# Optimization experiments

Measured on AMD Instinct MI355X. Metric: run time of the kernel, lower is better.

Reference implementation:

```python
import jax, jax.numpy as jnp
import numpy as np
from jax import lax

N, D, H = 4096, 256, 4


def setup_inputs() -> dict:
    key = jax.random.key(0)
    ks = jax.random.split(key, 6)
    x = jax.random.normal(ks[0], (1, 1, N, D), dtype=jnp.float32)
    adj = jax.random.randint(ks[1], (N, N), 0, 2, dtype=jnp.int32)
    conv_w = jax.random.normal(ks[2], (1, 1, 1, 1), dtype=jnp.float32)
    conv_b = jax.random.normal(ks[3], (1,), dtype=jnp.float32)
    # xavier_uniform on (H, 2D, 1) with gain 1.414
    limit = 1.414 * np.sqrt(6.0 / (2 * D + 1))
    a = jax.random.uniform(ks[4], (H, 2 * D, 1), minval=-limit, maxval=limit, dtype=jnp.float32)
    bias = jnp.zeros((D,), dtype=jnp.float32)
    return {"x": x, "adj": adj, "conv_w": conv_w, "conv_b": conv_b, "a": a, "bias": bias}


def reference(x, adj, conv_w, conv_b, a, bias):
    # 1x1 conv (NCHW / OIHW), preserves spatial dims
    h = lax.conv_general_dilated(x, conv_w, (1, 1), 'VALID',
                                 dimension_numbers=('NCHW', 'OIHW', 'NCHW'))
    h = h + conv_b[None, :, None, None]
    h = h[0, 0]                      # [N, D]
    d = h.shape[1]
    a1 = a[:, :d, 0]                 # [H, D]
    a2 = a[:, d:, 0]                 # [H, D]
    Wh1 = h @ a1.T                   # [N, H]
    Wh2 = h @ a2.T                   # [N, H]
    # e[k, i, j] = elu(Wh1[i, k] + Wh2[j, k])
    e = jax.nn.elu(Wh1.T[:, :, None] + Wh2.T[:, None, :])   # [H, N, N]
    att = jnp.where((adj > 0)[None, :, :], e, jnp.float32(-9e15))
    att = jax.nn.softmax(att, axis=-1)
    # dropout is inactive in eval mode (self.training=False)
    h_pass = jnp.einsum('hij,jd->hid', att, h).mean(axis=0)  # [N, D]
    out = jax.nn.elu(0.5 * h_pass + 0.5 * h)
    norm = jnp.maximum(jnp.linalg.norm(out, axis=1, keepdims=True), 1e-12)
    out = out / norm
    return out + bias
```

## Files before the change

kernel.cpp:

```cpp
#include <hip/hip_runtime.h>
#include <math.h>

#define NN 4096
#define DD 256
#define HH 4
#define SPLIT 8
#define BKG 64

typedef short short8 __attribute__((ext_vector_type(8)));
typedef float float4v __attribute__((ext_vector_type(4)));

__device__ __forceinline__ unsigned short f2bf(float f) {
  unsigned u = __float_as_uint(f);
  u += 0x7FFF + ((u >> 16) & 1);
  return (unsigned short)(u >> 16);
}
__device__ __forceinline__ unsigned f2bf_pk(float a, float b) {
  unsigned ua = __float_as_uint(a); ua += 0x7FFF + ((ua >> 16) & 1);
  unsigned ub = __float_as_uint(b); ub += 0x7FFF + ((ub >> 16) & 1);
  return __builtin_amdgcn_perm(ub, ua, 0x07060302);
}
__device__ __forceinline__ void gld16(void* lds, const void* gp) {
  __builtin_amdgcn_global_load_lds(
      (const __attribute__((address_space(1))) unsigned int*)gp,
      (__attribute__((address_space(3))) unsigned int*)lds, 16, 0, 0);
}

__global__ void k_zero(float* __restrict__ hp) {
  int idx = blockIdx.x * 256 + threadIdx.x;
  ((float4*)hp)[idx] = make_float4(0.f, 0.f, 0.f, 0.f);
}

__global__ __launch_bounds__(256) void k_pre(
    const float* __restrict__ x, const float* __restrict__ a,
    const float* __restrict__ cwp, const float* __restrict__ cbp,
    unsigned short* __restrict__ hbfT, float* __restrict__ Rpg,
    unsigned short* __restrict__ Ebf) {
  const int tid = threadIdx.x;
  const int bid = blockIdx.x;
  const float cw = cwp[0], cb = cbp[0];

  if (bid < 256) {
    __shared__ float t[64][65];
    const int j0 = (bid & 63) * 64, d0 = (bid >> 6) * 64;
    const int r = tid >> 4, c4 = tid & 15;
#pragma unroll
    for (int p = 0; p < 4; p++) {
      const int jj = p * 16 + r;
      const float4 v = *(const float4*)(x + (size_t)(j0 + jj) * DD + d0 + c4 * 4);
      t[jj][c4 * 4 + 0] = v.x * cw + cb;
      t[jj][c4 * 4 + 1] = v.y * cw + cb;
      t[jj][c4 * 4 + 2] = v.z * cw + cb;
      t[jj][c4 * 4 + 3] = v.w * cw + cb;
    }
    __syncthreads();
    const int jc = (tid & 15) * 4, db = tid >> 4;
#pragma unroll
    for (int p = 0; p < 4; p++) {
      const int dd = p * 16 + db;
      const unsigned l0 = f2bf(t[jc + 0][dd]);
      const unsigned l1 = f2bf(t[jc + 1][dd]);
      const unsigned l2 = f2bf(t[jc + 2][dd]);
      const unsigned l3 = f2bf(t[jc + 3][dd]);
      uint2 val;
      val.x = l0 | (l1 << 16);
      val.y = l2 | (l3 << 16);
      *(uint2*)(hbfT + (size_t)(d0 + dd) * NN + j0 + jc) = val;
    }
  } else {
    const int ln = tid >> 2, qd = (tid & 3) * 64;
    const int node = (bid - 256) * 64 + ln;
    float p1[HH] = {0.f, 0.f, 0.f, 0.f}, p2[HH] = {0.f, 0.f, 0.f, 0.f};
#pragma unroll
    for (int k = 0; k < 16; k++) {
      const int d = qd + k * 4;
      const float4 v = *(const float4*)(x + (size_t)node * DD + d);
      const float h0 = v.x * cw + cb, h1 = v.y * cw + cb;
      const float h2 = v.z * cw + cb, h3 = v.w * cw + cb;
#pragma unroll
      for (int h = 0; h < HH; h++) {
        const float4 a1 = *(const float4*)(a + h * 512 + d);
        const float4 a2 = *(const float4*)(a + h * 512 + 256 + d);
        p1[h] += h0 * a1.x + h1 * a1.y + h2 * a1.z + h3 * a1.w;
        p2[h] += h0 * a2.x + h1 * a2.y + h2 * a2.z + h3 * a2.w;
      }
    }
#pragma unroll
    for (int off = 1; off <= 2; off <<= 1) {
#pragma unroll
      for (int h = 0; h < HH; h++) {
        p1[h] += __shfl_xor(p1[h], off);
        p2[h] += __shfl_xor(p2[h], off);
      }
    }
    if ((tid & 3) == 0) {
#pragma unroll
      for (int h = 0; h < HH; h++) {
        Rpg[h * NN + node] = __expf(p1[h]);
        Ebf[h * NN + node] = f2bf(__expf(p2[h]));
      }
    }
  }
}

__global__ __launch_bounds__(256) void k_zw(
    const int* __restrict__ adj, const float* __restrict__ Rpg,
    const unsigned short* __restrict__ Ebf, unsigned short* __restrict__ Wm) {
  __shared__ float red[4][HH];
  __shared__ float sZi[HH];

  const int i = blockIdx.x;
  const int tid = threadIdx.x;
  const float C = 0.36787944117144233f;
  float Rp[HH], z[HH];
#pragma unroll
  for (int h = 0; h < HH; h++) {
    Rp[h] = Rpg[h * NN + i];
    z[h] = 0.f;
  }
  unsigned P[4][HH][2];
  const int4* arow = (const int4*)(adj + (size_t)i * NN);
#pragma unroll
  for (int k = 0; k < 4; k++) {
    const int j4 = tid + k * 256;
    const int4 av = arow[j4];
    const bool m0 = av.x > 0, m1 = av.y > 0, m2 = av.z > 0, m3 = av.w > 0;
#pragma unroll
    for (int h = 0; h < HH; h++) {
      const uint2 e2 = *(const uint2*)(Ebf + (size_t)h * NN + j4 * 4);
      const float E0 = __uint_as_float(e2.x << 16);
      const float E1 = __uint_as_float(e2.x & 0xffff0000u);
      const float E2 = __uint_as_float(e2.y << 16);
      const float E3 = __uint_as_float(e2.y & 0xffff0000u);
      float u, p0, p1, p2, p3;
      u = Rp[h] * E0; p0 = u > 1.f ? u : C * __expf(u);
      p0 = m0 ? p0 : 0.f;
      u = Rp[h] * E1; p1 = u > 1.f ? u : C * __expf(u);
      p1 = m1 ? p1 : 0.f;
      u = Rp[h] * E2; p2 = u > 1.f ? u : C * __expf(u);
      p2 = m2 ? p2 : 0.f;
      u = Rp[h] * E3; p3 = u > 1.f ? u : C * __expf(u);
      p3 = m3 ? p3 : 0.f;
      z[h] += (p0 + p1) + (p2 + p3);
      P[k][h][0] = f2bf_pk(p0, p1);
      P[k][h][1] = f2bf_pk(p2, p3);
    }
  }
#pragma unroll
  for (int h = 0; h < HH; h++) {
#pragma unroll
    for (int off = 32; off; off >>= 1) z[h] += __shfl_xor(z[h], off);
  }
  const int lane = tid & 63, wv = tid >> 6;
  if (lane == 0) {
#pragma unroll
    for (int h = 0; h < HH; h++) red[wv][h] = z[h];
  }
  __syncthreads();
  if (tid < HH) {
    const float zt = red[0][tid] + red[1][tid] + red[2][tid] + red[3][tid];
    sZi[tid] = zt > 0.f ? 0.25f / zt : 0.f;
  }
  __syncthreads();
  float Zi[HH];
#pragma unroll
  for (int h = 0; h < HH; h++) Zi[h] = sZi[h];

  unsigned* wrow = (unsigned*)(Wm + (size_t)i * NN);
#pragma unroll
  for (int k = 0; k < 4; k++) {
    const int j4 = tid + k * 256;
    float w0 = 0.f, w1 = 0.f, w2 = 0.f, w3 = 0.f;
#pragma unroll
    for (int h = 0; h < HH; h++) {
      const unsigned pa = P[k][h][0];
      const unsigned pb = P[k][h][1];
      w0 += __uint_as_float(pa << 16) * Zi[h];
      w1 += __uint_as_float(pa & 0xffff0000u) * Zi[h];
      w2 += __uint_as_float(pb << 16) * Zi[h];
      w3 += __uint_as_float(pb & 0xffff0000u) * Zi[h];
    }
    wrow[j4 * 2] = f2bf_pk(w0, w1);
    wrow[j4 * 2 + 1] = f2bf_pk(w2, w3);
  }
}

__global__ __launch_bounds__(256) void k_gemm(
    const unsigned short* __restrict__ Wm, const unsigned short* __restrict__ hbfT,
    float* __restrict__ hpOut, int useSplit) {
  __shared__ __align__(16) unsigned short sA[64 * 64];
  __shared__ __align__(16) unsigned short sB[256 * 64];
  const int tid = threadIdx.x;
  const int wv = tid >> 6, lane = tid & 63;
  const int m16 = lane & 15, q = lane >> 4, m7 = m16 & 7;
  const int rb = blockIdx.x >> 3, sp = blockIdx.x & 7;
  const int i0 = rb * 64;
  const int jlo = sp * (NN / SPLIT);
  const int lr = lane >> 3;
  const int lk8 = (lane & 7) ^ lr;

  float4v acc[4][4];
#pragma unroll
  for (int a = 0; a < 4; a++)
#pragma unroll
    for (int b = 0; b < 4; b++) acc[a][b] = (float4v)0.f;

  for (int kt = 0; kt < (NN / SPLIT) / BKG; kt++) {
    const int j0 = jlo + kt * BKG;
    __syncthreads();
#pragma unroll
    for (int t = 0; t < 2; t++) {
      const int r0 = wv * 16 + t * 8;
      gld16(sA + r0 * 64, Wm + (size_t)(i0 + r0 + lr) * NN + j0 + lk8 * 8);
    }
#pragma unroll
    for (int t = 0; t < 8; t++) {
      const int r0 = wv * 64 + t * 8;
      gld16(sB + r0 * 64, hbfT + (size_t)(r0 + lr) * NN + j0 + lk8 * 8);
    }
    __syncthreads();
#pragma unroll
    for (int ks = 0; ks < 2; ks++) {
      const int kp = ((ks * 4 + q) ^ m7) * 8;
      short8 aF[4], bF[4];
#pragma unroll
      for (int it = 0; it < 4; it++)
        aF[it] = *(const short8*)(sA + (it * 16 + m16) * 64 + kp);
#pragma unroll
      for (int dt = 0; dt < 4; dt++)
        bF[dt] = *(const short8*)(sB + (wv * 64 + dt * 16 + m16) * 64 + kp);
#pragma unroll
      for (int it = 0; it < 4; it++)
#pragma unroll
        for (int dt = 0; dt < 4; dt++)
          acc[it][dt] = __builtin_amdgcn_mfma_f32_16x16x32_bf16(aF[it], bF[dt], acc[it][dt], 0, 0, 0);
    }
  }

  if (useSplit) {
    float* base = hpOut + (size_t)sp * NN * DD;
#pragma unroll
    for (int it = 0; it < 4; it++)
#pragma unroll
      for (int dt = 0; dt < 4; dt++) {
        const int d = wv * 64 + dt * 16 + m16;
#pragma unroll
        for (int rg = 0; rg < 4; rg++)
          base[(size_t)(i0 + it * 16 + q * 4 + rg) * DD + d] = acc[it][dt][rg];
      }
  } else {
#pragma unroll
    for (int it = 0; it < 4; it++)
#pragma unroll
      for (int dt = 0; dt < 4; dt++) {
        const int d = wv * 64 + dt * 16 + m16;
#pragma unroll
        for (int rg = 0; rg < 4; rg++)
          atomicAdd(&hpOut[(size_t)(i0 + it * 16 + q * 4 + rg) * DD + d], acc[it][dt][rg]);
      }
  }
}

__global__ __launch_bounds__(256) void k_epi(
    const float* __restrict__ hp, int nsplit, const float* __restrict__ x,
    const float* __restrict__ cwp, const float* __restrict__ cbp,
    const float* __restrict__ bias, float* __restrict__ out) {
  const int lane = threadIdx.x & 63, wv = threadIdx.x >> 6;
  const int i = blockIdx.x * 4 + wv;
  const float cw = cwp[0], cb = cbp[0];
  const int d4 = lane * 4;
  float4 pv = make_float4(0.f, 0.f, 0.f, 0.f);
  for (int s = 0; s < nsplit; s++) {
    const float4 t = *(const float4*)(hp + (size_t)s * NN * DD + (size_t)i * DD + d4);
    pv.x += t.x; pv.y += t.y; pv.z += t.z; pv.w += t.w;
  }
  const float4 xv = *(const float4*)(x + (size_t)i * DD + d4);
  float4 v;
  v.x = 0.5f * pv.x + 0.5f * (xv.x * cw + cb);
  v.y = 0.5f * pv.y + 0.5f * (xv.y * cw + cb);
  v.z = 0.5f * pv.z + 0.5f * (xv.z * cw + cb);
  v.w = 0.5f * pv.w + 0.5f * (xv.w * cw + cb);
  v.x = v.x > 0.f ? v.x : expm1f(v.x);
  v.y = v.y > 0.f ? v.y : expm1f(v.y);
  v.z = v.z > 0.f ? v.z : expm1f(v.z);
  v.w = v.w > 0.f ? v.w : expm1f(v.w);
  float ss = v.x * v.x + v.y * v.y + v.z * v.z + v.w * v.w;
#pragma unroll
  for (int off = 32; off; off >>= 1) ss += __shfl_xor(ss, off);
  const float inv = 1.f / fmaxf(sqrtf(ss), 1e-12f);
  const float4 bv = *(const float4*)(bias + d4);
  float4 o;
  o.x = v.x * inv + bv.x;
  o.y = v.y * inv + bv.y;
  o.z = v.z * inv + bv.z;
  o.w = v.w * inv + bv.w;
  *(float4*)(out + (size_t)i * DD + d4) = o;
}

extern "C" void kernel_launch(void* const* d_in, const int* in_sizes, int n_in,
                              void* d_out, int out_size, void* d_ws, size_t ws_size,
                              hipStream_t stream) {
  const float* x = (const float*)d_in[0];
  const int* adj = (const int*)d_in[1];
  const float* cw = (const float*)d_in[2];
  const float* cb = (const float*)d_in[3];
  const float* a = (const float*)d_in[4];
  const float* bias = (const float*)d_in[5];
  float* out = (float*)d_out;
  float* ws = (float*)d_ws;

  float* Rpg = ws;
  unsigned short* Ebf = (unsigned short*)(ws + 16384);
  unsigned short* hbfT = (unsigned short*)(ws + 24576);
  unsigned short* Wm = (unsigned short*)(ws + 24576 + 524288);
  float* hp = ws + 24576 + 524288 + 8388608;

  const size_t needSplit =
      (size_t)(24576 + 524288 + 8388608 + (size_t)SPLIT * NN * DD) * 4;
  const int useSplit = (ws_size >= needSplit) ? 1 : 0;
  const int nsplit = useSplit ? SPLIT : 1;

  if (!useSplit) hipLaunchKernelGGL(k_zero, dim3(1024), dim3(256), 0, stream, hp);
  hipLaunchKernelGGL(k_pre, dim3(320), dim3(256), 0, stream, x, a, cw, cb, hbfT, Rpg, Ebf);
  hipLaunchKernelGGL(k_zw, dim3(NN), dim3(256), 0, stream, adj, Rpg, Ebf, Wm);
  hipLaunchKernelGGL(k_gemm, dim3(64 * SPLIT), dim3(256), 0, stream, Wm, hbfT, hp, useSplit);
  hipLaunchKernelGGL(k_epi, dim3(1024), dim3(256), 0, stream, hp, nsplit, x, cw, cb, bias, out);
}
```

Baseline: 167.6 us.

## Fuse split-K reduction and epilogue into GEMM via last-block counter

```diff
diff --git a/kernel.cpp b/kernel.cpp
--- a/kernel.cpp
+++ b/kernel.cpp
@@ -35,7 +35,7 @@
     const float* __restrict__ x, const float* __restrict__ a,
     const float* __restrict__ cwp, const float* __restrict__ cbp,
     unsigned short* __restrict__ hbfT, float* __restrict__ Rpg,
-    unsigned short* __restrict__ Ebf) {
+    unsigned short* __restrict__ Ebf, int* __restrict__ cnt) {
   const int tid = threadIdx.x;
   const int bid = blockIdx.x;
   const float cw = cwp[0], cb = cbp[0];
@@ -68,6 +68,7 @@
       *(uint2*)(hbfT + (size_t)(d0 + dd) * NN + j0 + jc) = val;
     }
   } else {
+    if (bid == 256 && tid < 64) cnt[tid] = 0;
     const int ln = tid >> 2, qd = (tid & 3) * 64;
     const int node = (bid - 256) * 64 + ln;
     float p1[HH] = {0.f, 0.f, 0.f, 0.f}, p2[HH] = {0.f, 0.f, 0.f, 0.f};
@@ -133,14 +134,10 @@
       const float E2 = __uint_as_float(e2.y << 16);
       const float E3 = __uint_as_float(e2.y & 0xffff0000u);
       float u, p0, p1, p2, p3;
-      u = Rp[h] * E0; p0 = u > 1.f ? u : C * __expf(u);
-      p0 = m0 ? p0 : 0.f;
-      u = Rp[h] * E1; p1 = u > 1.f ? u : C * __expf(u);
-      p1 = m1 ? p1 : 0.f;
-      u = Rp[h] * E2; p2 = u > 1.f ? u : C * __expf(u);
-      p2 = m2 ? p2 : 0.f;
-      u = Rp[h] * E3; p3 = u > 1.f ? u : C * __expf(u);
-      p3 = m3 ? p3 : 0.f;
+      u = Rp[h] * E0; p0 = u > 1.f ? u : C * __expf(u); p0 = m0 ? p0 : 0.f;
+      u = Rp[h] * E1; p1 = u > 1.f ? u : C * __expf(u); p1 = m1 ? p1 : 0.f;
+      u = Rp[h] * E2; p2 = u > 1.f ? u : C * __expf(u); p2 = m2 ? p2 : 0.f;
+      u = Rp[h] * E3; p3 = u > 1.f ? u : C * __expf(u); p3 = m3 ? p3 : 0.f;
       z[h] += (p0 + p1) + (p2 + p3);
       P[k][h][0] = f2bf_pk(p0, p1);
       P[k][h][1] = f2bf_pk(p2, p3);
@@ -187,7 +184,10 @@
 
 __global__ __launch_bounds__(256) void k_gemm(
     const unsigned short* __restrict__ Wm, const unsigned short* __restrict__ hbfT,
-    float* __restrict__ hpOut, int useSplit) {
+    float* __restrict__ hpOut, int useSplit,
+    const float* __restrict__ x, const float* __restrict__ cwp,
+    const float* __restrict__ cbp, const float* __restrict__ bias,
+    float* __restrict__ out, int* __restrict__ cnt) {
   __shared__ __align__(16) unsigned short sA[64 * 64];
   __shared__ __align__(16) unsigned short sB[256 * 64];
   const int tid = threadIdx.x;
@@ -248,6 +248,45 @@
         for (int rg = 0; rg < 4; rg++)
           base[(size_t)(i0 + it * 16 + q * 4 + rg) * DD + d] = acc[it][dt][rg];
       }
+    __threadfence();
+    __shared__ int lastFlag;
+    if (tid == 0) lastFlag = (atomicAdd(&cnt[rb], 1) == SPLIT - 1) ? 1 : 0;
+    __syncthreads();
+    if (lastFlag) {
+      __threadfence();
+      const float cw = cwp[0], cb = cbp[0];
+      const int d4 = lane * 4;
+      const float4 bv = *(const float4*)(bias + d4);
+      for (int r = wv; r < 64; r += 4) {
+        const int i = i0 + r;
+        float4 pv = make_float4(0.f, 0.f, 0.f, 0.f);
+#pragma unroll
+        for (int s = 0; s < SPLIT; s++) {
+          const float4 t = *(const float4*)(hpOut + (size_t)s * NN * DD + (size_t)i * DD + d4);
+          pv.x += t.x; pv.y += t.y; pv.z += t.z; pv.w += t.w;
+        }
+        const float4 xv = *(const float4*)(x + (size_t)i * DD + d4);
+        float4 v;
+        v.x = 0.5f * pv.x + 0.5f * (xv.x * cw + cb);
+        v.y = 0.5f * pv.y + 0.5f * (xv.y * cw + cb);
+        v.z = 0.5f * pv.z + 0.5f * (xv.z * cw + cb);
+        v.w = 0.5f * pv.w + 0.5f * (xv.w * cw + cb);
+        v.x = v.x > 0.f ? v.x : expm1f(v.x);
+        v.y = v.y > 0.f ? v.y : expm1f(v.y);
+        v.z = v.z > 0.f ? v.z : expm1f(v.z);
+        v.w = v.w > 0.f ? v.w : expm1f(v.w);
+        float ss = v.x * v.x + v.y * v.y + v.z * v.z + v.w * v.w;
+#pragma unroll
+        for (int off = 32; off; off >>= 1) ss += __shfl_xor(ss, off);
+        const float inv = 1.f / fmaxf(sqrtf(ss), 1e-12f);
+        float4 o;
+        o.x = v.x * inv + bv.x;
+        o.y = v.y * inv + bv.y;
+        o.z = v.z * inv + bv.z;
+        o.w = v.w * inv + bv.w;
+        *(float4*)(out + (size_t)i * DD + d4) = o;
+      }
+    }
   } else {
 #pragma unroll
     for (int it = 0; it < 4; it++)
@@ -314,15 +353,17 @@
   unsigned short* hbfT = (unsigned short*)(ws + 24576);
   unsigned short* Wm = (unsigned short*)(ws + 24576 + 524288);
   float* hp = ws + 24576 + 524288 + 8388608;
+  int* cnt = (int*)(ws + 24576 + 524288 + 8388608 + (size_t)SPLIT * NN * DD);
 
   const size_t needSplit =
-      (size_t)(24576 + 524288 + 8388608 + (size_t)SPLIT * NN * DD) * 4;
+      (size_t)(24576 + 524288 + 8388608 + (size_t)SPLIT * NN * DD + 64) * 4;
   const int useSplit = (ws_size >= needSplit) ? 1 : 0;
-  const int nsplit = useSplit ? SPLIT : 1;
 
   if (!useSplit) hipLaunchKernelGGL(k_zero, dim3(1024), dim3(256), 0, stream, hp);
-  hipLaunchKernelGGL(k_pre, dim3(320), dim3(256), 0, stream, x, a, cw, cb, hbfT, Rpg, Ebf);
+  hipLaunchKernelGGL(k_pre, dim3(320), dim3(256), 0, stream, x, a, cw, cb, hbfT, Rpg, Ebf, cnt);
   hipLaunchKernelGGL(k_zw, dim3(NN), dim3(256), 0, stream, adj, Rpg, Ebf, Wm);
-  hipLaunchKernelGGL(k_gemm, dim3(64 * SPLIT), dim3(256), 0, stream, Wm, hbfT, hp, useSplit);
-  hipLaunchKernelGGL(k_epi, dim3(1024), dim3(256), 0, stream, hp, nsplit, x, cw, cb, bias, out);
-}
+  hipLaunchKernelGGL(k_gemm, dim3(64 * SPLIT), dim3(256), 0, stream, Wm, hbfT, hp, useSplit,
+                     x, cw, cb, bias, out, cnt);
+  if (!useSplit)
+    hipLaunchKernelGGL(k_epi, dim3(1024), dim3(256), 0, stream, hp, 1, x, cw, cb, bias, out);
+}
```

After: 266.9 us. 1.59x slower.
